# Performance work log

Hardware: AMD Instinct MI355X
Metric: run time of the kernel (lower is better)

Reference implementation:

```python
import jax, jax.numpy as jnp
import numpy as np

B, S, E, H = 2, 2048, 1024, 16
D = E // H  # head_dim = 64


def setup_inputs() -> dict:
    key = jax.random.key(0)
    k1, k2, k3 = jax.random.split(key, 3)
    scale = 0.02  # GPT-2 init scale
    return {
        "hidden_states": jax.random.normal(k1, (B, S, E), dtype=jnp.float32),
        "c_attn_w": jax.random.normal(k2, (E, 3 * E), dtype=jnp.float32) * scale,
        "c_attn_b": jnp.zeros((3 * E,), dtype=jnp.float32),
        "c_proj_w": jax.random.normal(k3, (E, E), dtype=jnp.float32) * scale,
        "c_proj_b": jnp.zeros((E,), dtype=jnp.float32),
    }


def reference(hidden_states, c_attn_w, c_attn_b, c_proj_w, c_proj_b):
    # Conv1D: x @ W + b  -> qkv [B, S, 3E]
    qkv = hidden_states @ c_attn_w + c_attn_b
    q, k, v = jnp.split(qkv, 3, axis=-1)

    # split heads -> [B, H, S, D]
    def split_heads(t):
        return t.reshape(B, S, H, D).transpose(0, 2, 1, 3)

    q, k, v = split_heads(q), split_heads(k), split_heads(v)

    # naive full attention: QK^T / sqrt(D) -> softmax -> @ V
    attn_weights = jnp.einsum("bhqd,bhkd->bhqk", q, k) / jnp.sqrt(
        jnp.asarray(D, dtype=q.dtype)
    )
    attn_weights = jax.nn.softmax(attn_weights, axis=-1)
    attn_output = jnp.einsum("bhqk,bhkd->bhqd", attn_weights, v)

    # merge heads -> [B, S, E], then output projection
    attn_output = attn_output.transpose(0, 2, 1, 3).reshape(B, S, E)
    attn_output = attn_output @ c_proj_w + c_proj_b
    return attn_output
```

## Files before the change

### kernel.cpp

```cpp
#include <hip/hip_runtime.h>

#define SEQ 2048
#define EMB 1024
#define KDIM 1024
#define CF 0.180336880111113f

typedef __attribute__((ext_vector_type(8))) short short8_t;
typedef __attribute__((ext_vector_type(4))) float floatx4;
typedef __attribute__((ext_vector_type(4))) unsigned short ushort4_t;

#define GLOAD16(gp, lp)                                                        \
  __builtin_amdgcn_global_load_lds(                                            \
      (const __attribute__((address_space(1))) void*)(gp),                     \
      (__attribute__((address_space(3))) void*)(lp), 16, 0, 0)

#define WGBAR()                                   \
  do {                                            \
    __asm__ __volatile__("" ::: "memory");        \
    __builtin_amdgcn_s_barrier();                 \
    __asm__ __volatile__("" ::: "memory");        \
  } while (0)

static __device__ __forceinline__ unsigned short f2bf(float x) {
  unsigned int u = __float_as_uint(x);
  return (unsigned short)((u + 0x7fffu + ((u >> 16) & 1u)) >> 16);
}

__global__ __launch_bounds__(256) void conv_bf(
    const float* __restrict__ X, unsigned short* __restrict__ Y, int n4) {
  int i = blockIdx.x * 256 + threadIdx.x;
  if (i >= n4) return;
  float4 v = *(const float4*)&X[(size_t)i * 4];
  ushort4_t h = {f2bf(v.x), f2bf(v.y), f2bf(v.z), f2bf(v.w)};
  *(ushort4_t*)&Y[(size_t)i * 4] = h;
}

__global__ __launch_bounds__(256) void tconv(
    const float* __restrict__ W, unsigned short* __restrict__ T, int N, int K) {
  __shared__ float Tl[64][65];
  const int tid = threadIdx.x, lx = tid & 15, ly = tid >> 4;
  const int n0 = blockIdx.x * 64, k0 = blockIdx.y * 64;
#pragma unroll
  for (int u = 0; u < 4; ++u) {
    int r = u * 16 + ly;
    float4 v = *(const float4*)&W[(size_t)(k0 + r) * N + n0 + lx * 4];
    Tl[r][lx * 4 + 0] = v.x;
    Tl[r][lx * 4 + 1] = v.y;
    Tl[r][lx * 4 + 2] = v.z;
    Tl[r][lx * 4 + 3] = v.w;
  }
  __syncthreads();
#pragma unroll
  for (int u = 0; u < 4; ++u) {
    int n = u * 16 + ly;
    ushort4_t h;
#pragma unroll
    for (int v = 0; v < 4; ++v) h[v] = f2bf(Tl[lx * 4 + v][n]);
    *(ushort4_t*)&T[(size_t)(n0 + n) * K + k0 + lx * 4] = h;
  }
}

template <int MODE, int BN>
__global__ __launch_bounds__(256) void gemm_bf(
    const unsigned short* __restrict__ Ag, const unsigned short* __restrict__ Bg,
    const float* __restrict__ bias, float* __restrict__ outF,
    unsigned short* __restrict__ qk, unsigned short* __restrict__ vt, int N) {
  __shared__ __attribute__((aligned(16))) unsigned short Ah[128 * 32];
  __shared__ __attribute__((aligned(16))) unsigned short Bh[BN * 32];
  const int NJ = BN / 32;

  const int tid = threadIdx.x;
  const int w = tid >> 6, lane = tid & 63;
  const int quad = lane >> 4, c = lane & 15;
  const int bm = blockIdx.y * 128, bn = blockIdx.x * BN;
  const int wm = (w >> 1) * 64, wn = (w & 1) * (BN / 2);

  const unsigned short* gsrc = (w < 2) ? Ag : Bg;
  unsigned short* ldst = (w < 2) ? (Ah + (w & 1) * 64 * 32) : (Bh + (w & 1) * (BN / 2) * 32);
  const int rbase = (w < 2) ? (bm + (w & 1) * 64) : (bn + (w & 1) * (BN / 2));
  const int nloads = (w < 2) ? 4 : NJ;
  const int srow = lane >> 2;
  const int sblk = (lane & 3) ^ ((lane >> 3) & 3);
  const char* gp0 = (const char*)(gsrc + (size_t)(rbase + srow) * KDIM) + sblk * 16;

  floatx4 acc[4][NJ];
  const floatx4 z = {0.f, 0.f, 0.f, 0.f};
#pragma unroll
  for (int i = 0; i < 4; ++i)
#pragma unroll
    for (int j = 0; j < NJ; ++j) acc[i][j] = z;

  const int sw = (c >> 1) & 3;

  for (int k0 = 0; k0 < KDIM; k0 += 32) {
    __syncthreads();
    const char* gp = gp0 + k0 * 2;
    for (int i = 0; i < nloads; ++i) GLOAD16(gp + (size_t)i * 16 * (KDIM * 2), &ldst[i * 512]);
    __syncthreads();

    short8_t a[4], b[NJ];
#pragma unroll
    for (int i = 0; i < 4; ++i)
      a[i] = *(const short8_t*)&Ah[(wm + 16 * i + c) * 32 + ((quad ^ sw) * 8)];
#pragma unroll
    for (int j = 0; j < NJ; ++j)
      b[j] = *(const short8_t*)&Bh[(wn + 16 * j + c) * 32 + ((quad ^ sw) * 8)];
#pragma unroll
    for (int i = 0; i < 4; ++i)
#pragma unroll
      for (int j = 0; j < NJ; ++j)
        acc[i][j] = __builtin_amdgcn_mfma_f32_16x16x32_bf16(a[i], b[j], acc[i][j], 0, 0, 0);
  }

#pragma unroll
  for (int i = 0; i < 4; ++i) {
    const int r0 = bm + wm + 16 * i + quad * 4;
#pragma unroll
    for (int j = 0; j < NJ; ++j) {
      const int col = bn + wn + 16 * j + c;
      const float bv = bias[col];
      float v0 = acc[i][j][0] + bv, v1 = acc[i][j][1] + bv;
      float v2 = acc[i][j][2] + bv, v3 = acc[i][j][3] + bv;
      if (MODE == 0) {
        if (col < 1024) { v0 *= CF; v1 *= CF; v2 *= CF; v3 *= CF; }
        if (bn < 2048) {
          qk[(size_t)(r0 + 0) * 2048 + col] = f2bf(v0);
          qk[(size_t)(r0 + 1) * 2048 + col] = f2bf(v1);
          qk[(size_t)(r0 + 2) * 2048 + col] = f2bf(v2);
          qk[(size_t)(r0 + 3) * 2048 + col] = f2bf(v3);
        } else {
          const int c2 = col - 2048, hh = c2 >> 6, d = c2 & 63;
          const int bb = r0 >> 11, s = r0 & 2047;
          ushort4_t pk = {f2bf(v0), f2bf(v1), f2bf(v2), f2bf(v3)};
          *(ushort4_t*)&vt[((size_t)(bb * 16 + hh) * 64 + d) * 2048 + s] = pk;
        }
      } else {
        outF[(size_t)(r0 + 0) * N + col] = v0;
        outF[(size_t)(r0 + 1) * N + col] = v1;
        outF[(size_t)(r0 + 2) * N + col] = v2;
        outF[(size_t)(r0 + 3) * N + col] = v3;
      }
    }
  }
}

static __device__ __forceinline__ void stage_kv(
    int w, int srow, int sblkg, const unsigned short* __restrict__ gK,
    const unsigned short* __restrict__ gV, unsigned short* Kbuf,
    unsigned short* Vbuf, int jt) {
  if (w < 2) {
    const unsigned short* g0 = gK + (size_t)(jt * 64 + w * 32 + srow) * 2048 + sblkg * 8;
    unsigned short* l0 = &Kbuf[(w * 32) * 64];
#pragma unroll
    for (int i = 0; i < 4; ++i) GLOAD16(g0 + (size_t)i * 8 * 2048, &l0[i * 512]);
  } else {
    const unsigned short* g0 = gV + (size_t)((w - 2) * 32 + srow) * 2048 + jt * 64 + sblkg * 8;
    unsigned short* l0 = &Vbuf[((w - 2) * 32) * 64];
#pragma unroll
    for (int i = 0; i < 4; ++i) GLOAD16(g0 + (size_t)i * 8 * 2048, &l0[i * 512]);
  }
}

__global__ __launch_bounds__(256) void attn3(
    const unsigned short* __restrict__ qk, const unsigned short* __restrict__ vt,
    unsigned short* __restrict__ ao) {
  __shared__ __attribute__((aligned(16))) unsigned short Ks[2][64 * 64];
  __shared__ __attribute__((aligned(16))) unsigned short Vs[2][64 * 64];
  __shared__ __attribute__((aligned(16))) unsigned short Ps[4][32 * 64];

  const int tid = threadIdx.x;
  const int w = tid >> 6, lane = tid & 63, quad = lane >> 4, c = lane & 15;
  const int q0 = blockIdx.x * 128, h = blockIdx.y, b = blockIdx.z;

  short8_t qf[2][2];
  {
    const size_t rb = (size_t)b * SEQ + q0 + w * 32;
#pragma unroll
    for (int mi = 0; mi < 2; ++mi) {
      const size_t qr = (rb + mi * 16 + c) * 2048 + h * 64 + quad * 8;
      qf[mi][0] = *(const short8_t*)&qk[qr];
      qf[mi][1] = *(const short8_t*)&qk[qr + 32];
    }
  }
  __asm__ __volatile__("s_waitcnt vmcnt(0)" ::: "memory");

  floatx4 O[2][4], Osum[2];
  const floatx4 z = {0.f, 0.f, 0.f, 0.f};
#pragma unroll
  for (int mi = 0; mi < 2; ++mi) {
    Osum[mi] = z;
#pragma unroll
    for (int dg = 0; dg < 4; ++dg) O[mi][dg] = z;
  }
  short8_t ones;
#pragma unroll
  for (int e = 0; e < 8; ++e) ones[e] = (short)0x3F80;

  const int srow = lane >> 3;
  const int sblkg = (lane & 7) ^ (srow & 7);
  const unsigned short* gK = qk + (size_t)b * SEQ * 2048 + 1024 + h * 64;
  const unsigned short* gV = vt + (size_t)(b * 16 + h) * 64 * 2048;
  unsigned short* myPs = Ps[w];

  stage_kv(w, srow, sblkg, gK, gV, Ks[0], Vs[0], 0);

  for (int t = 0; t < 32; ++t) {
    const int cur = t & 1;
    WGBAR();
    stage_kv(w, srow, sblkg, gK, gV, Ks[cur ^ 1], Vs[cur ^ 1], (t + 1) & 31);
    __asm__ __volatile__("s_waitcnt vmcnt(4)" ::: "memory");
    WGBAR();
    const unsigned short* Kc = Ks[cur];
    const unsigned short* Vc = Vs[cur];

    floatx4 S[2][4];
#pragma unroll
    for (int mi = 0; mi < 2; ++mi)
#pragma unroll
      for (int jg = 0; jg < 4; ++jg) S[mi][jg] = z;
#pragma unroll
    for (int kq = 0; kq < 2; ++kq)
#pragma unroll
      for (int jg = 0; jg < 4; ++jg) {
        const int j = jg * 16 + c;
        short8_t kf = *(const short8_t*)&Kc[j * 64 + (((kq * 4 + quad) ^ (c & 7)) * 8)];
#pragma unroll
        for (int mi = 0; mi < 2; ++mi)
          S[mi][jg] = __builtin_amdgcn_mfma_f32_16x16x32_bf16(qf[mi][kq], kf, S[mi][jg], 0, 0, 0);
      }

#pragma unroll
    for (int mi = 0; mi < 2; ++mi)
#pragma unroll
      for (int r = 0; r < 4; ++r) {
        const int row = mi * 16 + quad * 4 + r;
        const int key = (row >> 1) & 7;
        unsigned short* pr = &myPs[row * 64 + (c & 7)];
#pragma unroll
        for (int jg = 0; jg < 4; ++jg) {
          float p = __builtin_amdgcn_exp2f(fminf(S[mi][jg][r], 88.0f));
          const int slot = (jg * 2 + (c >> 3)) ^ key;
          pr[slot * 8] = (unsigned short)(__float_as_uint(p) >> 16);
        }
      }
    __asm__ __volatile__("s_waitcnt lgkmcnt(0)" ::: "memory");

    short8_t pa[2][2];
#pragma unroll
    for (int mi = 0; mi < 2; ++mi) {
      const int row = mi * 16 + c;
      const int key = (row >> 1) & 7;
#pragma unroll
      for (int kq = 0; kq < 2; ++kq)
        pa[mi][kq] = *(const short8_t*)&myPs[row * 64 + (((kq * 4 + quad) ^ key) * 8)];
    }
#pragma unroll
    for (int mi = 0; mi < 2; ++mi) {
      Osum[mi] = __builtin_amdgcn_mfma_f32_16x16x32_bf16(pa[mi][0], ones, Osum[mi], 0, 0, 0);
      Osum[mi] = __builtin_amdgcn_mfma_f32_16x16x32_bf16(pa[mi][1], ones, Osum[mi], 0, 0, 0);
    }
#pragma unroll
    for (int kq = 0; kq < 2; ++kq)
#pragma unroll
      for (int dg = 0; dg < 4; ++dg) {
        const int d = dg * 16 + c;
        short8_t vf = *(const short8_t*)&Vc[d * 64 + (((kq * 4 + quad) ^ (c & 7)) * 8)];
#pragma unroll
        for (int mi = 0; mi < 2; ++mi)
          O[mi][dg] = __builtin_amdgcn_mfma_f32_16x16x32_bf16(pa[mi][kq], vf, O[mi][dg], 0, 0, 0);
      }
  }

  __asm__ __volatile__("s_waitcnt vmcnt(0)" ::: "memory");

#pragma unroll
  for (int mi = 0; mi < 2; ++mi) {
    float inv[4];
#pragma unroll
    for (int r = 0; r < 4; ++r) inv[r] = 1.0f / Osum[mi][r];
#pragma unroll
    for (int r = 0; r < 4; ++r) {
      const size_t row = (size_t)b * SEQ + q0 + w * 32 + mi * 16 + quad * 4 + r;
#pragma unroll
      for (int dg = 0; dg < 4; ++dg)
        ao[row * EMB + h * 64 + dg * 16 + c] = f2bf(O[mi][dg][r] * inv[r]);
    }
  }
}

extern "C" void kernel_launch(void* const* d_in, const int* in_sizes, int n_in,
                              void* d_out, int out_size, void* d_ws, size_t ws_size,
                              hipStream_t stream) {
  const float* hs = (const float*)d_in[0];
  const float* c_attn_w = (const float*)d_in[1];
  const float* c_attn_b = (const float*)d_in[2];
  const float* c_proj_w = (const float*)d_in[3];
  const float* c_proj_b = (const float*)d_in[4];
  float* out = (float*)d_out;

  char* ws = (char*)d_ws;
  unsigned short* hsb = (unsigned short*)(ws + 0);
  unsigned short* qk  = (unsigned short*)(ws + 8388608);
  unsigned short* vt  = (unsigned short*)(ws + 25165824);
  unsigned short* aob = (unsigned short*)(ws + 33554432);
  unsigned short* w1t = (unsigned short*)(ws + 41943040);
  unsigned short* w2t = (unsigned short*)(ws + 48234496);

  conv_bf<<<4096, 256, 0, stream>>>(hs, hsb, (2 * SEQ * EMB) / 4);
  tconv<<<dim3(48, 16), 256, 0, stream>>>(c_attn_w, w1t, 3 * EMB, EMB);
  tconv<<<dim3(16, 16), 256, 0, stream>>>(c_proj_w, w2t, EMB, EMB);
  gemm_bf<0, 128><<<dim3(24, 32), 256, 0, stream>>>(hsb, w1t, c_attn_b, nullptr, qk, vt, 3 * EMB);
  attn3<<<dim3(16, 16, 2), 256, 0, stream>>>(qk, vt, aob);
  gemm_bf<1, 64><<<dim3(16, 32), 256, 0, stream>>>(aob, w2t, c_proj_b, out, nullptr, nullptr, EMB);
}
```

Baseline: 201.1 us.

## Double GEMM K-step to 64 and transpose attention MFMA operands for packed P stores

The GEMM kernel now stages 64-wide K slices per iteration with an 8-way XOR swizzle, which halves the number of barrier pairs per tile but doubles LDS use. The attention kernel swaps MFMA operand order so S and O come out transposed (query along lanes). This lets P be written to LDS as packed 32-bit bf16 pairs and the output be stored as 4-element vectors. The fminf clamp on the exponent is dropped, and the softmax denominator is now read from one accumulator element.

```diff
diff --git a/kernel.cpp b/kernel.cpp
--- a/kernel.cpp
+++ b/kernel.cpp
@@ -65,8 +65,8 @@
     const unsigned short* __restrict__ Ag, const unsigned short* __restrict__ Bg,
     const float* __restrict__ bias, float* __restrict__ outF,
     unsigned short* __restrict__ qk, unsigned short* __restrict__ vt, int N) {
-  __shared__ __attribute__((aligned(16))) unsigned short Ah[128 * 32];
-  __shared__ __attribute__((aligned(16))) unsigned short Bh[BN * 32];
+  __shared__ __attribute__((aligned(16))) unsigned short Ah[128 * 64];
+  __shared__ __attribute__((aligned(16))) unsigned short Bh[BN * 64];
   const int NJ = BN / 32;
 
   const int tid = threadIdx.x;
@@ -76,11 +76,11 @@
   const int wm = (w >> 1) * 64, wn = (w & 1) * (BN / 2);
 
   const unsigned short* gsrc = (w < 2) ? Ag : Bg;
-  unsigned short* ldst = (w < 2) ? (Ah + (w & 1) * 64 * 32) : (Bh + (w & 1) * (BN / 2) * 32);
+  unsigned short* ldst = (w < 2) ? (Ah + (w & 1) * 64 * 64) : (Bh + (w & 1) * (BN / 2) * 64);
   const int rbase = (w < 2) ? (bm + (w & 1) * 64) : (bn + (w & 1) * (BN / 2));
-  const int nloads = (w < 2) ? 4 : NJ;
-  const int srow = lane >> 2;
-  const int sblk = (lane & 3) ^ ((lane >> 3) & 3);
+  const int nloads = (w < 2) ? 8 : (BN / 16);
+  const int srow = lane >> 3;
+  const int sblk = (lane & 7) ^ srow;
   const char* gp0 = (const char*)(gsrc + (size_t)(rbase + srow) * KDIM) + sblk * 16;
 
   floatx4 acc[4][NJ];
@@ -90,26 +90,30 @@
 #pragma unroll
     for (int j = 0; j < NJ; ++j) acc[i][j] = z;
 
-  const int sw = (c >> 1) & 3;
-
-  for (int k0 = 0; k0 < KDIM; k0 += 32) {
+  const int rk = c & 7;
+
+  for (int k0 = 0; k0 < KDIM; k0 += 64) {
     __syncthreads();
     const char* gp = gp0 + k0 * 2;
-    for (int i = 0; i < nloads; ++i) GLOAD16(gp + (size_t)i * 16 * (KDIM * 2), &ldst[i * 512]);
+    for (int i = 0; i < nloads; ++i) GLOAD16(gp + (size_t)i * 8 * (KDIM * 2), &ldst[i * 512]);
     __syncthreads();
 
-    short8_t a[4], b[NJ];
-#pragma unroll
-    for (int i = 0; i < 4; ++i)
-      a[i] = *(const short8_t*)&Ah[(wm + 16 * i + c) * 32 + ((quad ^ sw) * 8)];
-#pragma unroll
-    for (int j = 0; j < NJ; ++j)
-      b[j] = *(const short8_t*)&Bh[(wn + 16 * j + c) * 32 + ((quad ^ sw) * 8)];
-#pragma unroll
-    for (int i = 0; i < 4; ++i)
+#pragma unroll
+    for (int kq = 0; kq < 2; ++kq) {
+      const int oct = ((4 * kq + quad) ^ rk) * 8;
+      short8_t a[4], b[NJ];
+#pragma unroll
+      for (int i = 0; i < 4; ++i)
+        a[i] = *(const short8_t*)&Ah[(wm + 16 * i + c) * 64 + oct];
 #pragma unroll
       for (int j = 0; j < NJ; ++j)
-        acc[i][j] = __builtin_amdgcn_mfma_f32_16x16x32_bf16(a[i], b[j], acc[i][j], 0, 0, 0);
+        b[j] = *(const short8_t*)&Bh[(wn + 16 * j + c) * 64 + oct];
+#pragma unroll
+      for (int i = 0; i < 4; ++i)
+#pragma unroll
+        for (int j = 0; j < NJ; ++j)
+          acc[i][j] = __builtin_amdgcn_mfma_f32_16x16x32_bf16(a[i], b[j], acc[i][j], 0, 0, 0);
+    }
   }
 
 #pragma unroll
@@ -161,7 +165,7 @@
   }
 }
 
-__global__ __launch_bounds__(256) void attn3(
+__global__ __launch_bounds__(256) void attn4(
     const unsigned short* __restrict__ qk, const unsigned short* __restrict__ vt,
     unsigned short* __restrict__ ao) {
   __shared__ __attribute__((aligned(16))) unsigned short Ks[2][64 * 64];
@@ -171,6 +175,7 @@
   const int tid = threadIdx.x;
   const int w = tid >> 6, lane = tid & 63, quad = lane >> 4, c = lane & 15;
   const int q0 = blockIdx.x * 128, h = blockIdx.y, b = blockIdx.z;
+  const int rk = c & 7;
 
   short8_t qf[2][2];
   {
@@ -197,7 +202,7 @@
   for (int e = 0; e < 8; ++e) ones[e] = (short)0x3F80;
 
   const int srow = lane >> 3;
-  const int sblkg = (lane & 7) ^ (srow & 7);
+  const int sblkg = (lane & 7) ^ srow;
   const unsigned short* gK = qk + (size_t)b * SEQ * 2048 + 1024 + h * 64;
   const unsigned short* gV = vt + (size_t)(b * 16 + h) * 64 * 2048;
   unsigned short* myPs = Ps[w];
@@ -219,71 +224,69 @@
 #pragma unroll
       for (int jg = 0; jg < 4; ++jg) S[mi][jg] = z;
 #pragma unroll
-    for (int kq = 0; kq < 2; ++kq)
+    for (int kd = 0; kd < 2; ++kd) {
+      const int oct = ((4 * kd + quad) ^ rk) * 8;
 #pragma unroll
       for (int jg = 0; jg < 4; ++jg) {
-        const int j = jg * 16 + c;
-        short8_t kf = *(const short8_t*)&Kc[j * 64 + (((kq * 4 + quad) ^ (c & 7)) * 8)];
+        short8_t kf = *(const short8_t*)&Kc[(jg * 16 + c) * 64 + oct];
 #pragma unroll
         for (int mi = 0; mi < 2; ++mi)
-          S[mi][jg] = __builtin_amdgcn_mfma_f32_16x16x32_bf16(qf[mi][kq], kf, S[mi][jg], 0, 0, 0);
-      }
-
-#pragma unroll
-    for (int mi = 0; mi < 2; ++mi)
-#pragma unroll
-      for (int r = 0; r < 4; ++r) {
-        const int row = mi * 16 + quad * 4 + r;
-        const int key = (row >> 1) & 7;
-        unsigned short* pr = &myPs[row * 64 + (c & 7)];
-#pragma unroll
-        for (int jg = 0; jg < 4; ++jg) {
-          float p = __builtin_amdgcn_exp2f(fminf(S[mi][jg][r], 88.0f));
-          const int slot = (jg * 2 + (c >> 3)) ^ key;
-          pr[slot * 8] = (unsigned short)(__float_as_uint(p) >> 16);
+          S[mi][jg] = __builtin_amdgcn_mfma_f32_16x16x32_bf16(kf, qf[mi][kd], S[mi][jg], 0, 0, 0);
+      }
+    }
+
+#pragma unroll
+    for (int mi = 0; mi < 2; ++mi) {
+      const int qrow = (mi * 16 + c) * 64;
+#pragma unroll
+      for (int jg = 0; jg < 4; ++jg) {
+        float p0 = __builtin_amdgcn_exp2f(S[mi][jg][0]);
+        float p1 = __builtin_amdgcn_exp2f(S[mi][jg][1]);
+        float p2 = __builtin_amdgcn_exp2f(S[mi][jg][2]);
+        float p3 = __builtin_amdgcn_exp2f(S[mi][jg][3]);
+        unsigned int pk01 = (__float_as_uint(p1) & 0xFFFF0000u) | (__float_as_uint(p0) >> 16);
+        unsigned int pk23 = (__float_as_uint(p3) & 0xFFFF0000u) | (__float_as_uint(p2) >> 16);
+        const int jp0 = 8 * jg + 2 * quad;
+#pragma unroll
+        for (int u = 0; u < 2; ++u) {
+          const int jp = jp0 + u;
+          const int off = ((jp >> 2) ^ rk) * 8 + (jp & 3) * 2;
+          *(unsigned int*)&myPs[qrow + off] = u ? pk23 : pk01;
         }
       }
+    }
     __asm__ __volatile__("s_waitcnt lgkmcnt(0)" ::: "memory");
 
-    short8_t pa[2][2];
-#pragma unroll
-    for (int mi = 0; mi < 2; ++mi) {
-      const int row = mi * 16 + c;
-      const int key = (row >> 1) & 7;
-#pragma unroll
-      for (int kq = 0; kq < 2; ++kq)
-        pa[mi][kq] = *(const short8_t*)&myPs[row * 64 + (((kq * 4 + quad) ^ key) * 8)];
-    }
-#pragma unroll
-    for (int mi = 0; mi < 2; ++mi) {
-      Osum[mi] = __builtin_amdgcn_mfma_f32_16x16x32_bf16(pa[mi][0], ones, Osum[mi], 0, 0, 0);
-      Osum[mi] = __builtin_amdgcn_mfma_f32_16x16x32_bf16(pa[mi][1], ones, Osum[mi], 0, 0, 0);
-    }
-#pragma unroll
-    for (int kq = 0; kq < 2; ++kq)
+#pragma unroll
+    for (int kq = 0; kq < 2; ++kq) {
+      const int oct = ((4 * kq + quad) ^ rk) * 8;
+      short8_t pb[2];
+#pragma unroll
+      for (int mi = 0; mi < 2; ++mi) {
+        pb[mi] = *(const short8_t*)&myPs[(mi * 16 + c) * 64 + oct];
+        Osum[mi] = __builtin_amdgcn_mfma_f32_16x16x32_bf16(ones, pb[mi], Osum[mi], 0, 0, 0);
+      }
 #pragma unroll
       for (int dg = 0; dg < 4; ++dg) {
-        const int d = dg * 16 + c;
-        short8_t vf = *(const short8_t*)&Vc[d * 64 + (((kq * 4 + quad) ^ (c & 7)) * 8)];
+        short8_t vf = *(const short8_t*)&Vc[(dg * 16 + c) * 64 + oct];
 #pragma unroll
         for (int mi = 0; mi < 2; ++mi)
-          O[mi][dg] = __builtin_amdgcn_mfma_f32_16x16x32_bf16(pa[mi][kq], vf, O[mi][dg], 0, 0, 0);
-      }
+          O[mi][dg] = __builtin_amdgcn_mfma_f32_16x16x32_bf16(vf, pb[mi], O[mi][dg], 0, 0, 0);
+      }
+    }
   }
 
   __asm__ __volatile__("s_waitcnt vmcnt(0)" ::: "memory");
 
 #pragma unroll
   for (int mi = 0; mi < 2; ++mi) {
-    float inv[4];
-#pragma unroll
-    for (int r = 0; r < 4; ++r) inv[r] = 1.0f / Osum[mi][r];
-#pragma unroll
-    for (int r = 0; r < 4; ++r) {
-      const size_t row = (size_t)b * SEQ + q0 + w * 32 + mi * 16 + quad * 4 + r;
-#pragma unroll
-      for (int dg = 0; dg < 4; ++dg)
-        ao[row * EMB + h * 64 + dg * 16 + c] = f2bf(O[mi][dg][r] * inv[r]);
+    const float inv = 1.0f / Osum[mi][0];
+    const size_t row = (size_t)b * SEQ + q0 + w * 32 + mi * 16 + c;
+#pragma unroll
+    for (int dg = 0; dg < 4; ++dg) {
+      ushort4_t ov = {f2bf(O[mi][dg][0] * inv), f2bf(O[mi][dg][1] * inv),
+                      f2bf(O[mi][dg][2] * inv), f2bf(O[mi][dg][3] * inv)};
+      *(ushort4_t*)&ao[row * EMB + h * 64 + dg * 16 + quad * 4] = ov;
     }
   }
 }
@@ -310,6 +313,6 @@
   tconv<<<dim3(48, 16), 256, 0, stream>>>(c_attn_w, w1t, 3 * EMB, EMB);
   tconv<<<dim3(16, 16), 256, 0, stream>>>(c_proj_w, w2t, EMB, EMB);
   gemm_bf<0, 128><<<dim3(24, 32), 256, 0, stream>>>(hsb, w1t, c_attn_b, nullptr, qk, vt, 3 * EMB);
-  attn3<<<dim3(16, 16, 2), 256, 0, stream>>>(qk, vt, aob);
+  attn4<<<dim3(16, 16, 2), 256, 0, stream>>>(qk, vt, aob);
   gemm_bf<1, 64><<<dim3(16, 32), 256, 0, stream>>>(aob, w2t, c_proj_b, out, nullptr, nullptr, EMB);
 }
```

Result: no change. 197.6 us (-1.8%).
